# Optimization experiments

Measured on AMD Instinct MI355X. Metric: run time of the kernel, lower is better.

The kernel has to match this reference:

```python
import jax, jax.numpy as jnp
import numpy as np

K = 16
N_BLOCKS = 3
EPS = 1e-5  # nn.BatchNorm2d default eps


def setup_inputs() -> dict:
    key = jax.random.key(0)
    ks = jax.random.split(key, 4)
    b, n, c_out = 8, 4096, 64
    s = 0.1
    return {
        "xyz": jax.random.normal(ks[0], (b, 3, n), dtype=jnp.float32),
        "w1": jax.random.normal(ks[1], (c_out, 3), dtype=jnp.float32) * s,
        "b1": jnp.zeros((c_out,), jnp.float32),
        "w2": jax.random.normal(ks[2], (c_out, c_out), dtype=jnp.float32) * s,
        "b2": jnp.zeros((c_out,), jnp.float32),
        "gamma": jnp.ones((c_out,), jnp.float32),
        "beta": jnp.zeros((c_out,), jnp.float32),
    }


def _forward(xyz, w1, b1, w2, b2, gamma, beta):
    pts = jnp.transpose(xyz, (0, 2, 1))  # (b, n, 3)
    sq = jnp.sum(pts * pts, axis=-1)     # (b, n)
    # dist[b, i, j] = ||pts[b, j] - pts[b, i]||^2  (gram trick, avoids (b,n,n,3))
    dist = sq[:, :, None] + sq[:, None, :] - 2.0 * jnp.einsum('bic,bjc->bij', pts, pts)
    # NOTE: torch.topk defaults to LARGEST values -- faithful to the source code,
    # which (perhaps unintentionally) selects the k+1 FARTHEST points.
    _, idx = jax.lax.top_k(dist, K + 1)  # (b, n, K+1)
    idx = idx[:, :, 1:]                  # drop first, dilation=1 -> (b, n, K)
    # gather neighbor coords: nbr[b, i, j] = pts[b, idx[b, i, j]]
    nbr = jax.vmap(lambda p, i: p[i])(pts, idx)      # (b, n, K, 3)
    rel = nbr - pts[:, :, None, :]                    # relative coords (b, n, K, 3)
    g = jnp.transpose(rel, (0, 3, 2, 1))              # (b, 3, K, n)
    for blk in range(N_BLOCKS):
        w, bb = (w1, b1) if blk == 0 else (w2, b2)
        g = jnp.einsum('oc,bckn->bokn', w, g) + bb[None, :, None, None]
        if blk == N_BLOCKS - 1:
            return jnp.max(g, axis=2)                 # (b, c_out, n)
        # self.bn is the BatchNorm2d module (truthy) so BN is always applied;
        # fresh torch module is in training mode -> batch statistics.
        mu = jnp.mean(g, axis=(0, 2, 3), keepdims=True)
        var = jnp.mean((g - mu) ** 2, axis=(0, 2, 3), keepdims=True)
        g = (g - mu) * jax.lax.rsqrt(var + EPS)
        g = g * gamma[None, :, None, None] + beta[None, :, None, None]
        g = jax.nn.relu(g)


def reference(xyz, w1, b1, w2, b2, gamma, beta):
    return _forward(xyz, w1, b1, w2, b2, gamma, beta)
```

## Files before the change

### kernel.cpp

```cpp
#include <hip/hip_runtime.h>

typedef unsigned int u32;
typedef unsigned short u16;
typedef unsigned long long u64;
typedef __attribute__((ext_vector_type(8))) short bf16x8;
typedef __attribute__((ext_vector_type(4))) float f32x4;

#define REL_OFF   0
#define PTS4_OFF  1572864
#define ACC_OFF   1703936
#define EXT_OFF   1705360
#define EXT_END   1713552

__device__ __forceinline__ u32 bfh(float v){
  u32 x = __float_as_uint(v);
  return (x + 0x7FFFu + ((x >> 16) & 1u)) >> 16;
}
__device__ __forceinline__ void split2(float v, u16* hh, u16* hl){
  u32 h = bfh(v);
  float hif = __uint_as_float(h << 16);
  u32 l = bfh(v - hif);
  *hh = (u16)h; *hl = (u16)l;
}
__device__ __forceinline__ u32 cvt_pk_bf16(float a, float b){
  u32 r;
  asm("v_cvt_pk_bf16_f32 %0, %1, %2" : "=v"(r) : "v"(a), "v"(b));
  return r;
}

template<int N>
__device__ __forceinline__ float dpp_ror_f(float x){
  int r = __builtin_amdgcn_update_dpp(__float_as_int(x), __float_as_int(x),
                                      0x120 + N, 0xf, 0xf, false);
  return __int_as_float(r);
}
__device__ __forceinline__ float row_sum16(float x){
  x += dpp_ror_f<1>(x);
  x += dpp_ror_f<2>(x);
  x += dpp_ror_f<4>(x);
  x += dpp_ror_f<8>(x);
  return x;
}
__device__ __forceinline__ float row_max16(float x){
  x = fmaxf(x, dpp_ror_f<1>(x));
  x = fmaxf(x, dpp_ror_f<2>(x));
  x = fmaxf(x, dpp_ror_f<4>(x));
  x = fmaxf(x, dpp_ror_f<8>(x));
  return x;
}

__global__ __launch_bounds__(256) void prep_kernel(const float* __restrict__ xyz,
                                                   float4* __restrict__ pts4,
                                                   float* __restrict__ mom,
                                                   const float* __restrict__ w2,
                                                   u16* __restrict__ w2h,
                                                   u16* __restrict__ w2l,
                                                   float* __restrict__ gsum32,
                                                   float* __restrict__ gsq32,
                                                   int do_w2){
#pragma clang fp contract(off)
  int g = blockIdx.x*256 + threadIdx.x;
  if (g < 16) mom[g] = 0.0f;
  if (do_w2){
    if (g < 4096) split2(w2[g], &w2h[g], &w2l[g]);
    if (g < 2048) gsum32[g] = 0.0f;
    else if (g < 4096) gsq32[g-2048] = 0.0f;
  }
  int b = g >> 12, n = g & 4095;
  const float* xb = xyz + (size_t)b*12288;
  float x = xb[n], y = xb[4096+n], z = xb[8192+n];
  float sq = (x*x + y*y) + z*z;
  pts4[g] = make_float4(x,y,z,sq);
}

__global__ void w2prep_kernel(const float* __restrict__ w2,
                              u16* __restrict__ w2h, u16* __restrict__ w2l,
                              float* __restrict__ gsum32, float* __restrict__ gsq32){
  int i = blockIdx.x*256 + threadIdx.x;
  split2(w2[i], &w2h[i], &w2l[i]);
  if (i < 2048) gsum32[i] = 0.0f; else gsq32[i-2048] = 0.0f;
}

template<int N>
__device__ __forceinline__ void chain_insert_n(double* s, double key){
  #pragma unroll
  for (int t = N-1; t >= 1; --t)
    s[t] = fmax(s[t], fmin(s[t-1], key));
  s[0] = fmax(s[0], key);
}

__global__ __launch_bounds__(256) void knn_kernel(const float4* __restrict__ pts4,
                                                  float* __restrict__ rel,
                                                  float* __restrict__ mom){
#pragma clang fp contract(off)
  __shared__ double ring[4352];
  __shared__ float bmom[16];
  __shared__ u32 gate[32];
  u32* lA = (u32*)ring;
  u16* lB = (u16*)((char*)ring + 18048);
  const int tid  = threadIdx.x;
  const int lane = tid & 63;
  const int wave = tid >> 6;
  const int q    = lane & 31;
  const int h    = lane >> 5;
  const int sp   = wave*2 + h;
  const int blk  = blockIdx.x;
  const int b    = blk >> 7;
  const int q0   = (blk & 127) << 5;
  const float4* __restrict__ P = pts4 + ((size_t)b << 12);
  const float4* __restrict__ C = P + (sp << 9);
  const float4 me = P[q0 + q];
  if (tid < 16) bmom[tid] = 0.0f;
  if (tid < 32) gate[tid] = 0u;
  __syncthreads();

  double s[17];
  #pragma unroll
  for (int i=0;i<17;i++) s[i] = 0.0;
  const int base = tid*17;
  const int jg0 = sp << 9;
  u32 wr = 0, rd = 0;
  double pD_ = 0.0;
  const double kinv = 1.52587890625e-05;

  #define KEY48(u, J) ({                                              \
    float dot_ = (me.x*c[(u)].x + me.y*c[(u)].y) + me.z*c[(u)].z;     \
    float d_   = (me.w + c[(u)].w) - 2.0f*dot_;                       \
    u32 ub_ = __float_as_uint(d_);                                    \
    ub_ ^= ((u32)(((int)ub_) >> 31) | 0x80000000u);                   \
    (double)ub_ * 65536.0 + (double)(4095 - (J)); })

  {
    float4 c[8];
    #pragma unroll
    for (int u=0;u<8;u++) c[u] = C[u];
    chain_insert_n<1>(s, KEY48(0, jg0+0));
    chain_insert_n<2>(s, KEY48(1, jg0+1));
    chain_insert_n<3>(s, KEY48(2, jg0+2));
    chain_insert_n<4>(s, KEY48(3, jg0+3));
    chain_insert_n<5>(s, KEY48(4, jg0+4));
    chain_insert_n<6>(s, KEY48(5, jg0+5));
    chain_insert_n<7>(s, KEY48(6, jg0+6));
    chain_insert_n<8>(s, KEY48(7, jg0+7));
  }
  {
    float4 c[8];
    #pragma unroll
    for (int u=0;u<8;u++) c[u] = C[8+u];
    chain_insert_n< 9>(s, KEY48(0, jg0+ 8));
    chain_insert_n<10>(s, KEY48(1, jg0+ 9));
    chain_insert_n<11>(s, KEY48(2, jg0+10));
    chain_insert_n<12>(s, KEY48(3, jg0+11));
    chain_insert_n<13>(s, KEY48(4, jg0+12));
    chain_insert_n<14>(s, KEY48(5, jg0+13));
    chain_insert_n<15>(s, KEY48(6, jg0+14));
    chain_insert_n<16>(s, KEY48(7, jg0+15));
  }
  {
    float4 c[8];
    #pragma unroll
    for (int u=0;u<8;u++) c[u] = C[16+u];
    #pragma unroll
    for (int u=0;u<8;u++) chain_insert_n<17>(s, KEY48(u, jg0+16+u));
  }

  u32 lastpub = (u32)(s[16] * kinv);
  atomicMax(&gate[q], lastpub);
  u32 ob = lastpub;

  #define INSERT_STEP() {                                        \
    bool act = rd != wr;                                         \
    double key = act ? pD_ : 0.0;                                \
    rd += act;                                                   \
    pD_ = ring[base + (int)(rd & 15u)];                          \
    if (__any(key > s[16])) chain_insert_n<17>(s, key);          \
  }

  for (int g8 = 24; g8 < 512; g8 += 8){
    if (__any((int)(wr - rd) >= 9)){
      do { INSERT_STEP(); } while (__any(rd != wr));
      ob = (u32)(s[16] * kinv);
      if (ob > lastpub){ atomicMax(&gate[q], ob); lastpub = ob; }
    }
    float4 c[8];
    #pragma unroll
    for (int u=0;u<8;u++) c[u] = C[g8 + u];
    const u32 mb = max(gate[q], ob);
    const u32 ib = (mb >> 31) ? (mb ^ 0x80000000u) : ~mb;
    const float gmin = __uint_as_float(ib);
    const u32 wr0 = wr;
    #pragma unroll
    for (int u=0;u<8;u++){
      const int j = jg0 + g8 + u;
      float dot = (me.x*c[u].x + me.y*c[u].y) + me.z*c[u].z;
      float d   = (me.w + c[u].w) - 2.0f*dot;
      if (d >= gmin){
        u32 ub = __float_as_uint(d);
        ub ^= ((u32)(((int)ub) >> 31) | 0x80000000u);
        ring[base + (int)(wr & 15u)] = (double)ub * 65536.0 + (double)(4095 - j);
        wr++;
      }
    }
    if (wr != wr0) pD_ = ring[base + (int)(rd & 15u)];
  }
  while (__any(rd != wr)) INSERT_STEP();
  #undef INSERT_STEP
  #undef KEY48

  __syncthreads();
  #pragma unroll
  for (int i=0;i<17;i++){
    const int o = (sp*17 + i)*33 + q;
    u32 hi = (u32)(s[i] * kinv);
    u32 lo = (u32)(s[i] - (double)hi * 65536.0);
    lA[o] = hi;
    lB[o] = (u16)lo;
  }
  __syncthreads();

  {
    const int mq  = tid >> 3;
    const int sub = tid & 7;
    const float4 qp = P[q0 + mq];
    float* __restrict__ ro = rel + (size_t)((b << 12) + q0 + mq) * 48;
    float sm0=0,sm1=0,sm2=0,sm3=0,sm4=0,sm5=0,sm6=0,sm7=0,sm8=0;
    int p = 0;
    for (int r=0;r<17;r++){
      const int idx = (sub*17 + p)*33 + mq;
      u64 mine = ((u64)lA[idx] << 16) | lB[idx];
      u64 kmax = mine;
      #pragma unroll
      for (int off=1; off<8; off<<=1){
        u64 o2 = __shfl_xor(kmax, off);
        kmax = (o2 > kmax) ? o2 : kmax;
      }
      p += (mine == kmax);
      if (r > 0 && sub == 0){
        const int j = 4095 - (int)(u32)(kmax & 0xFFFFull);
        const float4 nb = P[j];
        const float rx = nb.x - qp.x;
        const float ry = nb.y - qp.y;
        const float rz = nb.z - qp.z;
        ro[(r-1)*3+0] = rx; ro[(r-1)*3+1] = ry; ro[(r-1)*3+2] = rz;
        sm0 += rx; sm1 += ry; sm2 += rz;
        sm3 += rx*rx; sm4 += rx*ry; sm5 += rx*rz;
        sm6 += ry*ry; sm7 += ry*rz; sm8 += rz*rz;
      }
    }
    #pragma unroll
    for (int off=8; off<64; off<<=1){
      sm0 += __shfl_xor(sm0, off); sm1 += __shfl_xor(sm1, off); sm2 += __shfl_xor(sm2, off);
      sm3 += __shfl_xor(sm3, off); sm4 += __shfl_xor(sm4, off); sm5 += __shfl_xor(sm5, off);
      sm6 += __shfl_xor(sm6, off); sm7 += __shfl_xor(sm7, off); sm8 += __shfl_xor(sm8, off);
    }
    if (lane == 0){
      atomicAdd(&bmom[0], sm0); atomicAdd(&bmom[1], sm1); atomicAdd(&bmom[2], sm2);
      atomicAdd(&bmom[3], sm3); atomicAdd(&bmom[4], sm4); atomicAdd(&bmom[5], sm5);
      atomicAdd(&bmom[6], sm6); atomicAdd(&bmom[7], sm7); atomicAdd(&bmom[8], sm8);
    }
  }
  __syncthreads();
  if (tid < 9) atomicAdd(&mom[tid], bmom[tid]);
}

__device__ __noinline__ void stats1_to_lds(int o, const float* __restrict__ mom,
    const float* __restrict__ w1, const float* __restrict__ b1,
    const float* __restrict__ gamma, const float* __restrict__ beta,
    float* a1){
  const float Minv = 1.0f / 524288.0f;
  float m0 = mom[0]*Minv, m1 = mom[1]*Minv, m2 = mom[2]*Minv;
  float cxx = mom[3]*Minv - m0*m0;
  float cxy = mom[4]*Minv - m0*m1;
  float cxz = mom[5]*Minv - m0*m2;
  float cyy = mom[6]*Minv - m1*m1;
  float cyz = mom[7]*Minv - m1*m2;
  float czz = mom[8]*Minv - m2*m2;
  float wx = w1[o*3+0], wy = w1[o*3+1], wz = w1[o*3+2];
  float mu  = wx*m0 + wy*m1 + wz*m2 + b1[o];
  float var = wx*wx*cxx + wy*wy*cyy + wz*wz*czz
            + 2.0f*(wx*wy*cxy + wx*wz*cxz + wy*wz*cyz);
  float istd = rsqrtf(var + 1e-5f);
  float sc = gamma[o]*istd;
  float t1 = beta[o] - mu*sc;
  a1[o*4+0] = wx*sc;
  a1[o*4+1] = wy*sc;
  a1[o*4+2] = wz*sc;
  a1[o*4+3] = fmaf(sc, b1[o], t1);
}

__device__ __forceinline__ void stage_H_core(int e, int half,
    float rx, float ry, float rz, const float* a1, u16* Hh, u16* Hl){
  const float4* A1 = (const float4*)a1;
  const int ch0 = half*32;
  #pragma unroll
  for (int i=0;i<32;i+=4){
    float g[4];
    #pragma unroll
    for (int r2=0;r2<4;r2++){
      float4 a = A1[ch0+i+r2];
      float t = fmaf(a.x, rx, fmaf(a.y, ry, fmaf(a.z, rz, a.w)));
      g[r2] = fmaxf(t, 0.0f);
    }
    u32 h01 = cvt_pk_bf16(g[0], g[1]);
    u32 h23 = cvt_pk_bf16(g[2], g[3]);
    float l0 = g[0] - __uint_as_float(h01 << 16);
    float l1 = g[1] - __uint_as_float(h01 & 0xFFFF0000u);
    float l2 = g[2] - __uint_as_float(h23 << 16);
    float l3 = g[3] - __uint_as_float(h23 & 0xFFFF0000u);
    u32 l01 = cvt_pk_bf16(l0, l1);
    u32 l23 = cvt_pk_bf16(l2, l3);
    *(uint2*)&Hh[e*72 + ch0 + i] = make_uint2(h01, h23);
    *(uint2*)&Hl[e*72 + ch0 + i] = make_uint2(l01, l23);
  }
}

#define MFMA6(dst, b_h0, b_h1, b_l0, b_l1)                                   \
  dst = __builtin_amdgcn_mfma_f32_16x16x32_bf16(aH0, b_h0, dst, 0,0,0);      \
  dst = __builtin_amdgcn_mfma_f32_16x16x32_bf16(aH1, b_h1, dst, 0,0,0);      \
  dst = __builtin_amdgcn_mfma_f32_16x16x32_bf16(aH0, b_l0, dst, 0,0,0);      \
  dst = __builtin_amdgcn_mfma_f32_16x16x32_bf16(aH1, b_l1, dst, 0,0,0);      \
  dst = __builtin_amdgcn_mfma_f32_16x16x32_bf16(aL0, b_h0, dst, 0,0,0);      \
  dst = __builtin_amdgcn_mfma_f32_16x16x32_bf16(aL1, b_h1, dst, 0,0,0);

#define LOAD_W_FRAGS()                                                        \
  const int rA = (wave*16 + col)*64 + quad*8;                                 \
  bf16x8 aH0 = *(const bf16x8*)&w2h[rA];                                      \
  bf16x8 aH1 = *(const bf16x8*)&w2h[rA+32];                                   \
  bf16x8 aL0 = *(const bf16x8*)&w2l[rA];                                      \
  bf16x8 aL1 = *(const bf16x8*)&w2l[rA+32];

__global__ __launch_bounds__(256) void pass2_mfma(
    const float* __restrict__ rel,
    const float* __restrict__ mom, const float* __restrict__ w1,
    const float* __restrict__ b1, const float* __restrict__ gamma,
    const float* __restrict__ beta,
    const u16* __restrict__ w2h, const u16* __restrict__ w2l,
    const float* __restrict__ b2,
    float* __restrict__ gsum32, float* __restrict__ gsq32){
  __shared__ alignas(16) u16 Hh[128*72], Hl[128*72];
  __shared__ float a1s[256];
  const int tid = threadIdx.x, blk = blockIdx.x;
  const int e = tid>>1, half = tid&1;
  size_t eg = (size_t)blk*128 + e;
  const float rx = rel[eg*3+0], ry = rel[eg*3+1], rz = rel[eg*3+2];
  if (tid < 64) stats1_to_lds(tid, mom, w1, b1, gamma, beta, a1s);
  __syncthreads();
  stage_H_core(e, half, rx, ry, rz, (const float*)a1s, Hh, Hl);
  __syncthreads();
  const int lane = tid & 63, wave = tid >> 6;
  const int col = lane & 15, quad = lane >> 4;
  LOAD_W_FRAGS()
  float b2v[4];
  #pragma unroll
  for (int r=0;r<4;r++) b2v[r] = b2[wave*16 + quad*4 + r];
  float ssum[4] = {0,0,0,0}, ssq[4] = {0,0,0,0};
  #pragma unroll
  for (int nt=0; nt<8; nt++){
    const int offB = (nt*16 + col)*72 + quad*8;
    bf16x8 bH0 = *(const bf16x8*)&Hh[offB];
    bf16x8 bH1 = *(const bf16x8*)&Hh[offB+32];
    bf16x8 bL0 = *(const bf16x8*)&Hl[offB];
    bf16x8 bL1 = *(const bf16x8*)&Hl[offB+32];
    f32x4 a = {0.f,0.f,0.f,0.f};
    MFMA6(a, bH0, bH1, bL0, bL1)
    #pragma unroll
    for (int r=0;r<4;r++){
      float t = a[r] + b2v[r];
      ssum[r] += t; ssq[r] += t*t;
    }
  }
  #pragma unroll
  for (int r=0;r<4;r++){
    ssum[r] = row_sum16(ssum[r]);
    ssq[r]  = row_sum16(ssq[r]);
  }
  if (col == 0){
    const int st = (blk & 31)*64;
    #pragma unroll
    for (int r=0;r<4;r++){
      int ch = wave*16 + quad*4 + r;
      atomicAdd(&gsum32[st+ch], ssum[r]);
      atomicAdd(&gsq32[st+ch],  ssq[r]);
    }
  }
}

__global__ __launch_bounds__(256) void pass3_mfma(
    const float* __restrict__ rel,
    const float* __restrict__ mom, const float* __restrict__ w1,
    const float* __restrict__ b1, const float* __restrict__ gamma,
    const float* __restrict__ beta,
    const u16* __restrict__ w2h, const u16* __restrict__ w2l,
    const float* __restrict__ b2,
    const float* __restrict__ gsum32, const float* __restrict__ gsq32,
    float* __restrict__ out){
  __shared__ alignas(16) u16 Hh[128*72], Hl[128*72];
  __shared__ float a1s[256];
  __shared__ float s2s[64], c2s[64];
  const int tid = threadIdx.x, blk = blockIdx.x;
  const int e = tid>>1, half = tid&1;
  size_t eg = (size_t)blk*128 + e;
  const float rx = rel[eg*3+0], ry = rel[eg*3+1], rz = rel[eg*3+2];
  if (tid < 64){
    stats1_to_lds(tid, mom, w1, b1, gamma, beta, a1s);
  } else if (tid < 128){
    const int o = tid - 64;
    float s = 0.f, q = 0.f;
    #pragma unroll
    for (int i=0;i<32;i++){ s += gsum32[i*64+o]; q += gsq32[i*64+o]; }
    const float Minv = 1.0f / 524288.0f;
    float mu  = s*Minv;
    float var = q*Minv - mu*mu;
    float istd = rsqrtf(var + 1e-5f);
    float sc = gamma[o]*istd;
    float t2 = beta[o] - mu*sc;
    s2s[o] = sc;
    c2s[o] = fmaf(sc, b2[o], t2);
  }
  __syncthreads();
  stage_H_core(e, half, rx, ry, rz, (const float*)a1s, Hh, Hl);
  __syncthreads();
  const int lane = tid & 63, wave = tid >> 6;
  const int col = lane & 15, quad = lane >> 4;
  LOAD_W_FRAGS()
  float s2v[4], c2v[4], b2v[4];
  #pragma unroll
  for (int r=0;r<4;r++){
    int ch = wave*16 + quad*4 + r;
    s2v[r] = s2s[ch]; c2v[r] = c2s[ch]; b2v[r] = b2[ch];
  }
  f32x4 acc[8];
  #pragma unroll
  for (int nt=0; nt<8; nt++){
    const int offB = (nt*16 + col)*72 + quad*8;
    bf16x8 bH0 = *(const bf16x8*)&Hh[offB];
    bf16x8 bH1 = *(const bf16x8*)&Hh[offB+32];
    bf16x8 bL0 = *(const bf16x8*)&Hl[offB];
    bf16x8 bL1 = *(const bf16x8*)&Hl[offB+32];
    f32x4 a = {0.f,0.f,0.f,0.f};
    MFMA6(a, bH0, bH1, bL0, bL1)
    acc[nt] = a;
  }
  __syncthreads();
  #pragma unroll
  for (int nt=0; nt<8; nt++){
    const int eo = nt*16 + col;
    const int ch0 = wave*16 + quad*4;
    float h0, h1, h2, h3;
    {
      float g0 = acc[nt][0] + b2v[0];
      float g1 = acc[nt][1] + b2v[1];
      float g2 = acc[nt][2] + b2v[2];
      float g3 = acc[nt][3] + b2v[3];
      h0 = fmaxf(fmaf(g0, s2v[0], c2v[0]), 0.0f);
      h1 = fmaxf(fmaf(g1, s2v[1], c2v[1]), 0.0f);
      h2 = fmaxf(fmaf(g2, s2v[2], c2v[2]), 0.0f);
      h3 = fmaxf(fmaf(g3, s2v[3], c2v[3]), 0.0f);
    }
    u32 h01 = cvt_pk_bf16(h0, h1);
    u32 h23 = cvt_pk_bf16(h2, h3);
    float l0 = h0 - __uint_as_float(h01 << 16);
    float l1 = h1 - __uint_as_float(h01 & 0xFFFF0000u);
    float l2 = h2 - __uint_as_float(h23 << 16);
    float l3 = h3 - __uint_as_float(h23 & 0xFFFF0000u);
    u32 l01 = cvt_pk_bf16(l0, l1);
    u32 l23 = cvt_pk_bf16(l2, l3);
    *(uint2*)&Hh[eo*72 + ch0] = make_uint2(h01, h23);
    *(uint2*)&Hl[eo*72 + ch0] = make_uint2(l01, l23);
  }
  __syncthreads();
  #pragma unroll
  for (int nt=0; nt<8; nt++){
    const int offB = (nt*16 + col)*72 + quad*8;
    bf16x8 bH0 = *(const bf16x8*)&Hh[offB];
    bf16x8 bH1 = *(const bf16x8*)&Hh[offB+32];
    bf16x8 bL0 = *(const bf16x8*)&Hl[offB];
    bf16x8 bL1 = *(const bf16x8*)&Hl[offB+32];
    f32x4 a = {0.f,0.f,0.f,0.f};
    MFMA6(a, bH0, bH1, bL0, bL1)
    acc[nt][0] = row_max16(a[0]+b2v[0]);
    acc[nt][1] = row_max16(a[1]+b2v[1]);
    acc[nt][2] = row_max16(a[2]+b2v[2]);
    acc[nt][3] = row_max16(a[3]+b2v[3]);
  }
  if (col == 0){
    const int bb = blk >> 9;
    const int n0 = (blk & 511) * 8;
    #pragma unroll
    for (int r=0;r<4;r++){
      const int ch = wave*16 + quad*4 + r;
      float* po = out + (((size_t)bb*64 + ch) << 12) + n0;
      f32x4 v0 = {acc[0][r], acc[1][r], acc[2][r], acc[3][r]};
      f32x4 v1 = {acc[4][r], acc[5][r], acc[6][r], acc[7][r]};
      *(f32x4*)po = v0;
      *((f32x4*)po + 1) = v1;
    }
  }
}

extern "C" void kernel_launch(void* const* d_in, const int* in_sizes, int n_in,
                              void* d_out, int out_size, void* d_ws, size_t ws_size,
                              hipStream_t stream){
  const float* xyz   = (const float*)d_in[0];
  const float* w1    = (const float*)d_in[1];
  const float* b1    = (const float*)d_in[2];
  const float* w2    = (const float*)d_in[3];
  const float* b2    = (const float*)d_in[4];
  const float* gamma = (const float*)d_in[5];
  const float* beta  = (const float*)d_in[6];
  float* out = (float*)d_out;
  float* ws  = (float*)d_ws;

  float*  rel    = ws + REL_OFF;
  float4* pts4   = (float4*)(ws + PTS4_OFF);
  float*  mom    = ws + ACC_OFF;

  const bool big = ws_size >= (size_t)EXT_END * sizeof(float);
  u16 *w2h, *w2l; float *gsum32, *gsq32;
  if (big){
    w2h    = (u16*)(ws + EXT_OFF);
    w2l    = (u16*)(ws + EXT_OFF + 2048);
    gsum32 = ws + EXT_OFF + 4096;
    gsq32  = ws + EXT_OFF + 6144;
  } else {
    w2h    = (u16*)(ws + PTS4_OFF);
    w2l    = (u16*)(ws + PTS4_OFF + 2048);
    gsum32 = ws + PTS4_OFF + 4096;
    gsq32  = ws + PTS4_OFF + 6144;
  }

  prep_kernel  <<<128,  256, 0, stream>>>(xyz, pts4, mom, w2, w2h, w2l,
                                          gsum32, gsq32, big ? 1 : 0);
  knn_kernel   <<<1024, 256, 0, stream>>>(pts4, rel, mom);
  if (!big)
    w2prep_kernel<<<16, 256, 0, stream>>>(w2, w2h, w2l, gsum32, gsq32);
  pass2_mfma   <<<4096, 256, 0, stream>>>(rel, mom, w1, b1, gamma, beta,
                                          w2h, w2l, b2, gsum32, gsq32);
  pass3_mfma   <<<4096, 256, 0, stream>>>(rel, mom, w1, b1, gamma, beta,
                                          w2h, w2l, b2, gsum32, gsq32, out);
}
```

Baseline: 266.4 us.

## Give each wave its own points and keep all W2 fragments in registers

```diff
diff --git a/kernel.cpp b/kernel.cpp
--- a/kernel.cpp
+++ b/kernel.cpp
@@ -5,6 +5,7 @@
 typedef unsigned long long u64;
 typedef __attribute__((ext_vector_type(8))) short bf16x8;
 typedef __attribute__((ext_vector_type(4))) float f32x4;
+typedef __attribute__((ext_vector_type(4))) u32 u32x4;
 
 #define REL_OFF   0
 #define PTS4_OFF  1572864
@@ -26,6 +27,9 @@
   u32 r;
   asm("v_cvt_pk_bf16_f32 %0, %1, %2" : "=v"(r) : "v"(a), "v"(b));
   return r;
+}
+__device__ __forceinline__ bf16x8 as_bf16x8(u32x4 v){
+  union { u32x4 u; bf16x8 b; } c; c.u = v; return c.b;
 }
 
 template<int N>
@@ -288,46 +292,55 @@
   a1[o*4+3] = fmaf(sc, b1[o], t1);
 }
 
-__device__ __forceinline__ void stage_H_core(int e, int half,
-    float rx, float ry, float rz, const float* a1, u16* Hh, u16* Hl){
-  const float4* A1 = (const float4*)a1;
-  const int ch0 = half*32;
-  #pragma unroll
-  for (int i=0;i<32;i+=4){
-    float g[4];
-    #pragma unroll
-    for (int r2=0;r2<4;r2++){
-      float4 a = A1[ch0+i+r2];
-      float t = fmaf(a.x, rx, fmaf(a.y, ry, fmaf(a.z, rz, a.w)));
-      g[r2] = fmaxf(t, 0.0f);
-    }
-    u32 h01 = cvt_pk_bf16(g[0], g[1]);
-    u32 h23 = cvt_pk_bf16(g[2], g[3]);
-    float l0 = g[0] - __uint_as_float(h01 << 16);
-    float l1 = g[1] - __uint_as_float(h01 & 0xFFFF0000u);
-    float l2 = g[2] - __uint_as_float(h23 << 16);
-    float l3 = g[3] - __uint_as_float(h23 & 0xFFFF0000u);
-    u32 l01 = cvt_pk_bf16(l0, l1);
-    u32 l23 = cvt_pk_bf16(l2, l3);
-    *(uint2*)&Hh[e*72 + ch0 + i] = make_uint2(h01, h23);
-    *(uint2*)&Hl[e*72 + ch0 + i] = make_uint2(l01, l23);
-  }
-}
-
-#define MFMA6(dst, b_h0, b_h1, b_l0, b_l1)                                   \
-  dst = __builtin_amdgcn_mfma_f32_16x16x32_bf16(aH0, b_h0, dst, 0,0,0);      \
-  dst = __builtin_amdgcn_mfma_f32_16x16x32_bf16(aH1, b_h1, dst, 0,0,0);      \
-  dst = __builtin_amdgcn_mfma_f32_16x16x32_bf16(aH0, b_l0, dst, 0,0,0);      \
-  dst = __builtin_amdgcn_mfma_f32_16x16x32_bf16(aH1, b_l1, dst, 0,0,0);      \
-  dst = __builtin_amdgcn_mfma_f32_16x16x32_bf16(aL0, b_h0, dst, 0,0,0);      \
-  dst = __builtin_amdgcn_mfma_f32_16x16x32_bf16(aL1, b_h1, dst, 0,0,0);
-
-#define LOAD_W_FRAGS()                                                        \
-  const int rA = (wave*16 + col)*64 + quad*8;                                 \
-  bf16x8 aH0 = *(const bf16x8*)&w2h[rA];                                      \
-  bf16x8 aH1 = *(const bf16x8*)&w2h[rA+32];                                   \
-  bf16x8 aL0 = *(const bf16x8*)&w2l[rA];                                      \
-  bf16x8 aL1 = *(const bf16x8*)&w2l[rA+32];
+__device__ __forceinline__ void stage2_reg(
+    const float* a1s, int quad,
+    float rx0,float ry0,float rz0, float rx1,float ry1,float rz1,
+    bf16x8 bh0[2], bf16x8 bl0[2], bf16x8 bh1[2], bf16x8 bl1[2]){
+  const float4* A1 = (const float4*)a1s;
+  #pragma unroll
+  for (int hf=0; hf<2; hf++){
+    const int c0 = quad*8 + hf*32;
+    u32x4 H0,L0,H1,L1;
+    #pragma unroll
+    for (int p=0;p<4;p++){
+      float4 aA = A1[c0+2*p];
+      float4 aB = A1[c0+2*p+1];
+      float gA0 = fmaxf(fmaf(aA.x,rx0,fmaf(aA.y,ry0,fmaf(aA.z,rz0,aA.w))),0.f);
+      float gB0 = fmaxf(fmaf(aB.x,rx0,fmaf(aB.y,ry0,fmaf(aB.z,rz0,aB.w))),0.f);
+      float gA1 = fmaxf(fmaf(aA.x,rx1,fmaf(aA.y,ry1,fmaf(aA.z,rz1,aA.w))),0.f);
+      float gB1 = fmaxf(fmaf(aB.x,rx1,fmaf(aB.y,ry1,fmaf(aB.z,rz1,aB.w))),0.f);
+      u32 h0 = cvt_pk_bf16(gA0,gB0);
+      u32 h1 = cvt_pk_bf16(gA1,gB1);
+      float lA0 = gA0 - __uint_as_float(h0<<16);
+      float lB0 = gB0 - __uint_as_float(h0 & 0xFFFF0000u);
+      float lA1 = gA1 - __uint_as_float(h1<<16);
+      float lB1 = gB1 - __uint_as_float(h1 & 0xFFFF0000u);
+      H0[p]=h0; H1[p]=h1;
+      L0[p]=cvt_pk_bf16(lA0,lB0); L1[p]=cvt_pk_bf16(lA1,lB1);
+    }
+    bh0[hf]=as_bf16x8(H0); bl0[hf]=as_bf16x8(L0);
+    bh1[hf]=as_bf16x8(H1); bl1[hf]=as_bf16x8(L1);
+  }
+}
+
+#define MFMA6G(dst, A0,A1_,A2,A3, b_h0,b_h1,b_l0,b_l1)                        \
+  dst = __builtin_amdgcn_mfma_f32_16x16x32_bf16(A0,  b_h0, dst, 0,0,0);       \
+  dst = __builtin_amdgcn_mfma_f32_16x16x32_bf16(A1_, b_h1, dst, 0,0,0);       \
+  dst = __builtin_amdgcn_mfma_f32_16x16x32_bf16(A0,  b_l0, dst, 0,0,0);       \
+  dst = __builtin_amdgcn_mfma_f32_16x16x32_bf16(A1_, b_l1, dst, 0,0,0);       \
+  dst = __builtin_amdgcn_mfma_f32_16x16x32_bf16(A2,  b_h0, dst, 0,0,0);       \
+  dst = __builtin_amdgcn_mfma_f32_16x16x32_bf16(A3,  b_h1, dst, 0,0,0);
+
+#define LOAD_W_ALL()                                                          \
+  bf16x8 wH0[4], wH1[4], wL0[4], wL1[4];                                      \
+  _Pragma("unroll")                                                           \
+  for (int g=0; g<4; g++){                                                    \
+    const int rA = (g*16 + col)*64 + quad*8;                                  \
+    wH0[g] = *(const bf16x8*)&w2h[rA];                                        \
+    wH1[g] = *(const bf16x8*)&w2h[rA+32];                                     \
+    wL0[g] = *(const bf16x8*)&w2l[rA];                                        \
+    wL1[g] = *(const bf16x8*)&w2l[rA+32];                                     \
+  }
 
 __global__ __launch_bounds__(256) void pass2_mfma(
     const float* __restrict__ rel,
@@ -337,50 +350,44 @@
     const u16* __restrict__ w2h, const u16* __restrict__ w2l,
     const float* __restrict__ b2,
     float* __restrict__ gsum32, float* __restrict__ gsq32){
-  __shared__ alignas(16) u16 Hh[128*72], Hl[128*72];
   __shared__ float a1s[256];
   const int tid = threadIdx.x, blk = blockIdx.x;
-  const int e = tid>>1, half = tid&1;
-  size_t eg = (size_t)blk*128 + e;
-  const float rx = rel[eg*3+0], ry = rel[eg*3+1], rz = rel[eg*3+2];
-  if (tid < 64) stats1_to_lds(tid, mom, w1, b1, gamma, beta, a1s);
-  __syncthreads();
-  stage_H_core(e, half, rx, ry, rz, (const float*)a1s, Hh, Hl);
-  __syncthreads();
   const int lane = tid & 63, wave = tid >> 6;
   const int col = lane & 15, quad = lane >> 4;
-  LOAD_W_FRAGS()
-  float b2v[4];
-  #pragma unroll
-  for (int r=0;r<4;r++) b2v[r] = b2[wave*16 + quad*4 + r];
-  float ssum[4] = {0,0,0,0}, ssq[4] = {0,0,0,0};
-  #pragma unroll
-  for (int nt=0; nt<8; nt++){
-    const int offB = (nt*16 + col)*72 + quad*8;
-    bf16x8 bH0 = *(const bf16x8*)&Hh[offB];
-    bf16x8 bH1 = *(const bf16x8*)&Hh[offB+32];
-    bf16x8 bL0 = *(const bf16x8*)&Hl[offB];
-    bf16x8 bL1 = *(const bf16x8*)&Hl[offB+32];
+  const size_t eg0 = (size_t)blk*128 + (wave*2)*16 + col;
+  const float rx0 = rel[eg0*3+0], ry0 = rel[eg0*3+1], rz0 = rel[eg0*3+2];
+  const float rx1 = rel[(eg0+16)*3+0], ry1 = rel[(eg0+16)*3+1], rz1 = rel[(eg0+16)*3+2];
+  if (tid < 64) stats1_to_lds(tid, mom, w1, b1, gamma, beta, a1s);
+  __syncthreads();
+  bf16x8 bh0[2], bl0[2], bh1[2], bl1[2];
+  stage2_reg(a1s, quad, rx0,ry0,rz0, rx1,ry1,rz1, bh0,bl0,bh1,bl1);
+  LOAD_W_ALL()
+  f32x4 acc0[4], acc1[4];
+  #pragma unroll
+  for (int g=0; g<4; g++){
     f32x4 a = {0.f,0.f,0.f,0.f};
-    MFMA6(a, bH0, bH1, bL0, bL1)
-    #pragma unroll
-    for (int r=0;r<4;r++){
-      float t = a[r] + b2v[r];
-      ssum[r] += t; ssq[r] += t*t;
-    }
-  }
-  #pragma unroll
-  for (int r=0;r<4;r++){
-    ssum[r] = row_sum16(ssum[r]);
-    ssq[r]  = row_sum16(ssq[r]);
-  }
-  if (col == 0){
-    const int st = (blk & 31)*64;
-    #pragma unroll
-    for (int r=0;r<4;r++){
-      int ch = wave*16 + quad*4 + r;
-      atomicAdd(&gsum32[st+ch], ssum[r]);
-      atomicAdd(&gsq32[st+ch],  ssq[r]);
+    MFMA6G(a, wH0[g],wH1[g],wL0[g],wL1[g], bh0[0],bh0[1],bl0[0],bl0[1])
+    acc0[g] = a;
+    f32x4 b = {0.f,0.f,0.f,0.f};
+    MFMA6G(b, wH0[g],wH1[g],wL0[g],wL1[g], bh1[0],bh1[1],bl1[0],bl1[1])
+    acc1[g] = b;
+  }
+  const int st = (blk & 31)*64;
+  #pragma unroll
+  for (int g=0; g<4; g++){
+    float4 b2v = *(const float4*)&b2[g*16 + quad*4];
+    #pragma unroll
+    for (int r=0; r<4; r++){
+      float bb = (r==0)?b2v.x:(r==1)?b2v.y:(r==2)?b2v.z:b2v.w;
+      float t0 = acc0[g][r] + bb;
+      float t1 = acc1[g][r] + bb;
+      float s = row_sum16(t0 + t1);
+      float q = row_sum16(t0*t0 + t1*t1);
+      if (col == 0){
+        int ch = g*16 + quad*4 + r;
+        atomicAdd(&gsum32[st+ch], s);
+        atomicAdd(&gsq32[st+ch],  q);
+      }
     }
   }
 }
@@ -397,10 +404,13 @@
   __shared__ alignas(16) u16 Hh[128*72], Hl[128*72];
   __shared__ float a1s[256];
   __shared__ float s2s[64], c2s[64];
+  __shared__ float mx[512];
   const int tid = threadIdx.x, blk = blockIdx.x;
-  const int e = tid>>1, half = tid&1;
-  size_t eg = (size_t)blk*128 + e;
-  const float rx = rel[eg*3+0], ry = rel[eg*3+1], rz = rel[eg*3+2];
+  const int lane = tid & 63, wave = tid >> 6;
+  const int col = lane & 15, quad = lane >> 4;
+  const size_t eg0 = (size_t)blk*128 + (wave*2)*16 + col;
+  const float rx0 = rel[eg0*3+0], ry0 = rel[eg0*3+1], rz0 = rel[eg0*3+2];
+  const float rx1 = rel[(eg0+16)*3+0], ry1 = rel[(eg0+16)*3+1], rz1 = rel[(eg0+16)*3+2];
   if (tid < 64){
     stats1_to_lds(tid, mom, w1, b1, gamma, beta, a1s);
   } else if (tid < 128){
@@ -418,83 +428,82 @@
     c2s[o] = fmaf(sc, b2[o], t2);
   }
   __syncthreads();
-  stage_H_core(e, half, rx, ry, rz, (const float*)a1s, Hh, Hl);
-  __syncthreads();
-  const int lane = tid & 63, wave = tid >> 6;
-  const int col = lane & 15, quad = lane >> 4;
-  LOAD_W_FRAGS()
-  float s2v[4], c2v[4], b2v[4];
-  #pragma unroll
-  for (int r=0;r<4;r++){
-    int ch = wave*16 + quad*4 + r;
-    s2v[r] = s2s[ch]; c2v[r] = c2s[ch]; b2v[r] = b2[ch];
-  }
-  f32x4 acc[8];
-  #pragma unroll
-  for (int nt=0; nt<8; nt++){
-    const int offB = (nt*16 + col)*72 + quad*8;
-    bf16x8 bH0 = *(const bf16x8*)&Hh[offB];
-    bf16x8 bH1 = *(const bf16x8*)&Hh[offB+32];
-    bf16x8 bL0 = *(const bf16x8*)&Hl[offB];
-    bf16x8 bL1 = *(const bf16x8*)&Hl[offB+32];
+  bf16x8 bh0[2], bl0[2], bh1[2], bl1[2];
+  stage2_reg(a1s, quad, rx0,ry0,rz0, rx1,ry1,rz1, bh0,bl0,bh1,bl1);
+  LOAD_W_ALL()
+  f32x4 acc0[4], acc1[4];
+  #pragma unroll
+  for (int g=0; g<4; g++){
     f32x4 a = {0.f,0.f,0.f,0.f};
-    MFMA6(a, bH0, bH1, bL0, bL1)
-    acc[nt] = a;
-  }
-  __syncthreads();
-  #pragma unroll
-  for (int nt=0; nt<8; nt++){
-    const int eo = nt*16 + col;
-    const int ch0 = wave*16 + quad*4;
-    float h0, h1, h2, h3;
-    {
-      float g0 = acc[nt][0] + b2v[0];
-      float g1 = acc[nt][1] + b2v[1];
-      float g2 = acc[nt][2] + b2v[2];
-      float g3 = acc[nt][3] + b2v[3];
-      h0 = fmaxf(fmaf(g0, s2v[0], c2v[0]), 0.0f);
-      h1 = fmaxf(fmaf(g1, s2v[1], c2v[1]), 0.0f);
-      h2 = fmaxf(fmaf(g2, s2v[2], c2v[2]), 0.0f);
-      h3 = fmaxf(fmaf(g3, s2v[3], c2v[3]), 0.0f);
-    }
-    u32 h01 = cvt_pk_bf16(h0, h1);
-    u32 h23 = cvt_pk_bf16(h2, h3);
-    float l0 = h0 - __uint_as_float(h01 << 16);
-    float l1 = h1 - __uint_as_float(h01 & 0xFFFF0000u);
-    float l2 = h2 - __uint_as_float(h23 << 16);
-    float l3 = h3 - __uint_as_float(h23 & 0xFFFF0000u);
-    u32 l01 = cvt_pk_bf16(l0, l1);
-    u32 l23 = cvt_pk_bf16(l2, l3);
-    *(uint2*)&Hh[eo*72 + ch0] = make_uint2(h01, h23);
-    *(uint2*)&Hl[eo*72 + ch0] = make_uint2(l01, l23);
-  }
-  __syncthreads();
-  #pragma unroll
-  for (int nt=0; nt<8; nt++){
-    const int offB = (nt*16 + col)*72 + quad*8;
-    bf16x8 bH0 = *(const bf16x8*)&Hh[offB];
-    bf16x8 bH1 = *(const bf16x8*)&Hh[offB+32];
-    bf16x8 bL0 = *(const bf16x8*)&Hl[offB];
-    bf16x8 bL1 = *(const bf16x8*)&Hl[offB+32];
-    f32x4 a = {0.f,0.f,0.f,0.f};
-    MFMA6(a, bH0, bH1, bL0, bL1)
-    acc[nt][0] = row_max16(a[0]+b2v[0]);
-    acc[nt][1] = row_max16(a[1]+b2v[1]);
-    acc[nt][2] = row_max16(a[2]+b2v[2]);
-    acc[nt][3] = row_max16(a[3]+b2v[3]);
-  }
-  if (col == 0){
-    const int bb = blk >> 9;
-    const int n0 = (blk & 511) * 8;
-    #pragma unroll
-    for (int r=0;r<4;r++){
-      const int ch = wave*16 + quad*4 + r;
-      float* po = out + (((size_t)bb*64 + ch) << 12) + n0;
-      f32x4 v0 = {acc[0][r], acc[1][r], acc[2][r], acc[3][r]};
-      f32x4 v1 = {acc[4][r], acc[5][r], acc[6][r], acc[7][r]};
-      *(f32x4*)po = v0;
-      *((f32x4*)po + 1) = v1;
-    }
+    MFMA6G(a, wH0[g],wH1[g],wL0[g],wL1[g], bh0[0],bh0[1],bl0[0],bl0[1])
+    acc0[g] = a;
+    f32x4 b = {0.f,0.f,0.f,0.f};
+    MFMA6G(b, wH0[g],wH1[g],wL0[g],wL1[g], bh1[0],bh1[1],bl1[0],bl1[1])
+    acc1[g] = b;
+  }
+  float4 b2v4[4], s2v4[4], c2v4[4];
+  #pragma unroll
+  for (int g=0; g<4; g++){
+    b2v4[g] = *(const float4*)&b2[g*16 + quad*4];
+    s2v4[g] = *(const float4*)&s2s[g*16 + quad*4];
+    c2v4[g] = *(const float4*)&c2s[g*16 + quad*4];
+  }
+  #pragma unroll
+  for (int t=0; t<2; t++){
+    const int e = (wave*2 + t)*16 + col;
+    #pragma unroll
+    for (int g=0; g<4; g++){
+      f32x4 a = t ? acc1[g] : acc0[g];
+      float h0 = fmaxf(fmaf(a[0]+b2v4[g].x, s2v4[g].x, c2v4[g].x), 0.0f);
+      float h1 = fmaxf(fmaf(a[1]+b2v4[g].y, s2v4[g].y, c2v4[g].y), 0.0f);
+      float h2 = fmaxf(fmaf(a[2]+b2v4[g].z, s2v4[g].z, c2v4[g].z), 0.0f);
+      float h3 = fmaxf(fmaf(a[3]+b2v4[g].w, s2v4[g].w, c2v4[g].w), 0.0f);
+      u32 h01 = cvt_pk_bf16(h0, h1);
+      u32 h23 = cvt_pk_bf16(h2, h3);
+      float l0 = h0 - __uint_as_float(h01 << 16);
+      float l1 = h1 - __uint_as_float(h01 & 0xFFFF0000u);
+      float l2 = h2 - __uint_as_float(h23 << 16);
+      float l3 = h3 - __uint_as_float(h23 & 0xFFFF0000u);
+      u32 l01 = cvt_pk_bf16(l0, l1);
+      u32 l23 = cvt_pk_bf16(l2, l3);
+      const int ch0 = g*16 + quad*4;
+      *(uint2*)&Hh[e*72 + ch0] = make_uint2(h01, h23);
+      *(uint2*)&Hl[e*72 + ch0] = make_uint2(l01, l23);
+    }
+  }
+  __syncthreads();
+  #pragma unroll
+  for (int t=0; t<2; t++){
+    const int e = (wave*2 + t)*16 + col;
+    bf16x8 ch_[2], cl_[2];
+    #pragma unroll
+    for (int hf=0; hf<2; hf++){
+      ch_[hf] = *(const bf16x8*)&Hh[e*72 + quad*8 + hf*32];
+      cl_[hf] = *(const bf16x8*)&Hl[e*72 + quad*8 + hf*32];
+    }
+    #pragma unroll
+    for (int g=0; g<4; g++){
+      f32x4 a = {0.f,0.f,0.f,0.f};
+      MFMA6G(a, wH0[g],wH1[g],wL0[g],wL1[g], ch_[0],ch_[1],cl_[0],cl_[1])
+      f32x4 mm;
+      mm[0] = row_max16(a[0] + b2v4[g].x);
+      mm[1] = row_max16(a[1] + b2v4[g].y);
+      mm[2] = row_max16(a[2] + b2v4[g].z);
+      mm[3] = row_max16(a[3] + b2v4[g].w);
+      if (col == g)
+        *(f32x4*)&mx[(wave*2 + t)*64 + g*16 + quad*4] = mm;
+    }
+  }
+  __syncthreads();
+  if (tid < 128){
+    const int ch = tid >> 1, hf = tid & 1;
+    f32x4 v;
+    v[0] = mx[(hf*4+0)*64 + ch];
+    v[1] = mx[(hf*4+1)*64 + ch];
+    v[2] = mx[(hf*4+2)*64 + ch];
+    v[3] = mx[(hf*4+3)*64 + ch];
+    float* po = out + (((size_t)(blk>>9)*64 + ch) << 12) + (blk & 511)*8 + hf*4;
+    *(f32x4*)po = v;
   }
 }
 
```

After: 353.6 us. 32.7% more time.
